# Kernel optimization log

Measured on AMD Instinct MI355X. Metric: run time of the kernel, lower is better.

## Reference

```python
import jax, jax.numpy as jnp
from jax import lax
import numpy as np

S, D, L, H, C = 128, 3, 16, 512, 10
B, T = 32, 16384


def setup_inputs() -> dict:
    key = jax.random.key(0)
    ks = jax.random.split(key, 6)
    x = jax.random.normal(ks[0], (B, D, T), dtype=jnp.float32)
    shapelets = jax.random.normal(ks[1], (S, 1, D, L), dtype=jnp.float32)  # OIHW, one per shapelet
    W1 = jax.random.normal(ks[2], (H, S), dtype=jnp.float32) * (1.0 / np.sqrt(S))
    b1 = jnp.zeros((H,), dtype=jnp.float32)
    W2 = jax.random.normal(ks[3], (C, H), dtype=jnp.float32) * (1.0 / np.sqrt(H))
    b2 = jnp.zeros((C,), dtype=jnp.float32)
    return {"x": x, "shapelets": shapelets, "W1": W1, "b1": b1, "W2": W2, "b2": b2}


def reference(x, shapelets, W1, b1, W2, b2):
    # x: [B, D, T] -> [B, 1, D, T]; kernels slide only over time (full-height conv).
    x4 = x[:, None, :, :]
    dn = ("NCHW", "OIHW", "NCHW")
    ones_k = jnp.ones((1, 1, shapelets.shape[2], shapelets.shape[3]), dtype=x.dtype)
    # ||window||^2 per sliding window: [B, 1, 1, Tout]
    window_square = lax.conv_general_dilated(x4 * x4, ones_k, (1, 1), "VALID", dimension_numbers=dn)
    # all cross-correlations in one grouped conv: [B, S, 1, Tout]
    cross_corr = lax.conv_general_dilated(x4, shapelets, (1, 1), "VALID", dimension_numbers=dn)
    shapelet_square = jnp.sum(shapelets * shapelets, axis=(1, 2, 3))  # [S]
    # squared distance per (shapelet, window), min-reduced over windows
    dist = window_square + shapelet_square[None, :, None, None] - 2.0 * cross_corr  # [B, S, 1, Tout]
    distance = jnp.min(dist, axis=(2, 3))  # [B, S]
    h = jax.nn.relu(distance @ W1.T + b1)
    classification = h @ W2.T + b2
    return (distance, classification)
```

## Files before the change

kernel.cpp:

```cpp
#include <hip/hip_runtime.h>

#define Bn 32
#define Tn 16384
#define Ln 16
#define Sn 128
#define Hn 512
#define Cn 10
#define Kn 48
#define TOUT 16369
#define CH 1024
#define NCH 16
#define XBP 8224

typedef short  s16x8  __attribute__((ext_vector_type(8)));
typedef float  f32x16 __attribute__((ext_vector_type(16)));

static __device__ __forceinline__ unsigned short f2bf(float f) {
    union { float f; unsigned int u; } v; v.f = f;
    unsigned int r = v.u + 0x7FFF + ((v.u >> 16) & 1);
    return (unsigned short)(r >> 16);
}
static __device__ __forceinline__ unsigned int pk(float a, float b) {
    return (unsigned int)f2bf(a) | ((unsigned int)f2bf(b) << 16);
}
static __device__ __forceinline__ unsigned int pk2(unsigned short a, unsigned short b) {
    return (unsigned int)a | ((unsigned int)b << 16);
}
static __device__ __forceinline__ s16x8 mk_a(uint4 t) {
    union { uint4 u; s16x8 v; } c; c.u = t; return c.v;
}

__global__ __launch_bounds__(256) void prep_kernel(const float* __restrict__ x,
                                                   const float* __restrict__ sh,
                                                   unsigned int* __restrict__ shb,
                                                   float* __restrict__ shsq_g,
                                                   float* __restrict__ wsqT,
                                                   unsigned int* __restrict__ xg) {
    const int tid = threadIdx.x;
    if (blockIdx.x == 0) {
        if (tid < Sn) {
            const float4* r4 = (const float4*)(sh + tid * Kn);
            float v[48]; float q = 0.f;
            #pragma unroll
            for (int c = 0; c < 12; ++c) {
                const float4 t = r4[c];
                v[4*c] = t.x; v[4*c+1] = t.y; v[4*c+2] = t.z; v[4*c+3] = t.w;
                q = fmaf(t.x, t.x, q); q = fmaf(t.y, t.y, q);
                q = fmaf(t.z, t.z, q); q = fmaf(t.w, t.w, q);
            }
            shsq_g[tid] = q;
            uint4* dst = (uint4*)(shb + tid * 24);
            #pragma unroll
            for (int c = 0; c < 6; ++c) {
                uint4 o;
                o.x = pk(-2.f*v[8*c  ], -2.f*v[8*c+1]);
                o.y = pk(-2.f*v[8*c+2], -2.f*v[8*c+3]);
                o.z = pk(-2.f*v[8*c+4], -2.f*v[8*c+5]);
                o.w = pk(-2.f*v[8*c+6], -2.f*v[8*c+7]);
                dst[c] = o;
            }
        } else {
            const int idx = tid - 128;
            const uint4 z = {0u, 0u, 0u, 0u};
            for (int r = idx; r < 768; r += 128) {
                uint4* d = (uint4*)(xg + r * XBP + 8192);
                #pragma unroll
                for (int q = 0; q < 8; ++q) d[q] = z;
            }
        }
        return;
    }
    const int bid = blockIdx.x - 1;
    const int b    = bid >> 4;
    const int t0   = ((bid & 15) << 10) + 4 * tid;
    float q[4] = {0.f, 0.f, 0.f, 0.f};
    #pragma unroll
    for (int ch = 0; ch < 3; ++ch) {
        const float* xs = x + (b * 3 + ch) * Tn + t0;
        float wv[20];
        if (t0 + 20 <= Tn) {
            const float4* x4 = (const float4*)xs;
            #pragma unroll
            for (int c = 0; c < 5; ++c) {
                const float4 t = x4[c];
                wv[4*c] = t.x; wv[4*c+1] = t.y; wv[4*c+2] = t.z; wv[4*c+3] = t.w;
            }
        } else {
            #pragma unroll
            for (int k = 0; k < 20; ++k) wv[k] = (t0 + k < Tn) ? xs[k] : 0.f;
        }
        float s = 0.f;
        #pragma unroll
        for (int l = 0; l < 16; ++l) s = fmaf(wv[l], wv[l], s);
        q[0] += s;
        #pragma unroll
        for (int j = 1; j < 4; ++j) {
            s = s - wv[j-1]*wv[j-1] + wv[j+15]*wv[j+15];
            q[j] += s;
        }
        unsigned short bf[20];
        #pragma unroll
        for (int k = 0; k < 20; ++k) bf[k] = f2bf(wv[k]);
        unsigned int* xrow = xg + (b * 24 + ch) * XBP + (t0 >> 1);
        #pragma unroll
        for (int p = 0; p < 8; ++p) {
            uint2 o = { pk2(bf[p], bf[p+1]), pk2(bf[p+2], bf[p+3]) };
            *(uint2*)(xrow + p * 3 * XBP) = o;
        }
    }
    const int r0 = t0 & 15, col = t0 >> 4;
    float* wrow = wsqT + b * (16 * 1024) + col;
    #pragma unroll
    for (int c = 0; c < 4; ++c)
        wrow[(r0 + c) * 1024] = (t0 + c >= TOUT) ? 1e30f : q[c];
}

__global__ __launch_bounds__(256, 3) void dist_kernel(const unsigned int* __restrict__ shb,
                                                      const float* __restrict__ shsq_g,
                                                      const float* __restrict__ wsqT,
                                                      const unsigned int* __restrict__ xg,
                                                      float* __restrict__ partial) {
    __shared__ float wavemin[4 * 64];

    const int tid   = threadIdx.x;
    const int b     = blockIdx.x >> 5;
    const int rem   = blockIdx.x & 31;
    const int chunk = rem >> 1;
    const int half  = rem & 1;
    const int tb    = chunk * CH;
    const int lane  = tid & 63;
    const int w     = tid >> 6;
    const int n     = lane & 31;
    const int h     = lane >> 5;

    s16x8 bfr[3][2];
    float shsqv[2];
    #pragma unroll
    for (int st = 0; st < 2; ++st) {
        const int s = half * 64 + st * 32 + n;
        const uint4* base = (const uint4*)(shb + s * 24);
        #pragma unroll
        for (int kk = 0; kk < 3; ++kk)
            bfr[kk][st] = mk_a(base[kk * 2 + h]);
        shsqv[st] = shsq_g[s];
    }

    float mcol[2] = {1e30f, 1e30f};
    const f32x16 zero16 = {0.f, 0.f, 0.f, 0.f, 0.f, 0.f, 0.f, 0.f,
                           0.f, 0.f, 0.f, 0.f, 0.f, 0.f, 0.f, 0.f};
    const unsigned int* xgb  = xg + b * 24 * XBP + (tb >> 1);
    const float*        wrowb = wsqT + b * (16 * 1024) + (tb >> 4);

    #pragma unroll 2
    for (int rr = 0; rr < 8; ++rr) {
        const int tau = 8 * w + rr;
        const int i   = (tau & 15) + ((tau >> 4) << 9);
        const int p   = i & 7;
        const unsigned int* arow = xgb + p * 3 * XBP + (((i & ~7) >> 1) + 8 * n + 4 * h);
        const s16x8 a0 = mk_a(*(const uint4*)(arow));
        const s16x8 a1 = mk_a(*(const uint4*)(arow + XBP));
        const s16x8 a2 = mk_a(*(const uint4*)(arow + 2 * XBP));

        f32x16 acc[2];
        #pragma unroll
        for (int st = 0; st < 2; ++st) {
            acc[st] = __builtin_amdgcn_mfma_f32_32x32x16_bf16(a0, bfr[0][st], zero16, 0, 0, 0);
            acc[st] = __builtin_amdgcn_mfma_f32_32x32x16_bf16(a1, bfr[1][st], acc[st], 0, 0, 0);
            acc[st] = __builtin_amdgcn_mfma_f32_32x32x16_bf16(a2, bfr[2][st], acc[st], 0, 0, 0);
        }

        const float* wrow = wrowb + (i & 15) * 1024 + ((i >> 9) << 5);
        float4 wq[4];
        #pragma unroll
        for (int q = 0; q < 4; ++q)
            wq[q] = *(const float4*)(wrow + 8 * q + 4 * h);

        #pragma unroll
        for (int st = 0; st < 2; ++st)
            #pragma unroll
            for (int reg = 0; reg < 16; reg += 2) {
                const float u = acc[st][reg]     + ((const float*)&wq[reg >> 2])[(reg & 3)];
                const float v = acc[st][reg + 1] + ((const float*)&wq[reg >> 2])[(reg & 3) + 1];
                mcol[st] = fminf(fminf(mcol[st], u), v);
            }
    }

    #pragma unroll
    for (int st = 0; st < 2; ++st) {
        float mm = mcol[st] + shsqv[st];
        mm = fminf(mm, __shfl_xor(mm, 32, 64));
        if (h == 0) wavemin[w * 64 + st * 32 + n] = mm;
    }
    __syncthreads();
    if (tid < 64) {
        const float mm = fminf(fminf(wavemin[tid], wavemin[64 + tid]),
                               fminf(wavemin[128 + tid], wavemin[192 + tid]));
        partial[(b * NCH + chunk) * Sn + half * 64 + tid] = mm;
    }
}

__global__ __launch_bounds__(512) void mlp_kernel(const float* __restrict__ partial,
                                                  const float* __restrict__ W1,
                                                  const float* __restrict__ b1,
                                                  const float* __restrict__ W2,
                                                  const float* __restrict__ b2,
                                                  float* __restrict__ out) {
    __shared__ float pmin[4][Sn];
    __shared__ float db[Sn];
    __shared__ float hb[Hn];
    __shared__ float part[Cn][32];
    const int b = blockIdx.x, tid = threadIdx.x;

    {
        const int s = tid & 127, g = tid >> 7;
        const float* pp = partial + (b * NCH + g * 4) * Sn + s;
        float m = pp[0];
        #pragma unroll
        for (int c = 1; c < 4; ++c) m = fminf(m, pp[c * Sn]);
        pmin[g][s] = m;
    }
    __syncthreads();
    if (tid < Sn) {
        const float m = fminf(fminf(pmin[0][tid], pmin[1][tid]),
                              fminf(pmin[2][tid], pmin[3][tid]));
        db[tid] = m;
        out[b * Sn + tid] = m;
    }
    __syncthreads();

    float a = b1[tid];
    const float4* w1r = (const float4*)(W1 + tid * Sn);
    const float4* dbv = (const float4*)db;
    #pragma unroll
    for (int i = 0; i < Sn / 4; ++i) {
        const float4 wv = w1r[i];
        const float4 dv = dbv[i];
        a = fmaf(dv.x, wv.x, a); a = fmaf(dv.y, wv.y, a);
        a = fmaf(dv.z, wv.z, a); a = fmaf(dv.w, wv.w, a);
    }
    hb[tid] = fmaxf(a, 0.0f);
    __syncthreads();

    if (tid < Cn * 32) {
        const int c = tid >> 5, p = tid & 31;
        float acc = 0.f;
        #pragma unroll
        for (int i = 0; i < Hn / 32; ++i)
            acc = fmaf(hb[p + 32 * i], W2[c * Hn + p + 32 * i], acc);
        part[c][p] = acc;
    }
    __syncthreads();
    if (tid < Cn) {
        float acc = b2[tid];
        #pragma unroll
        for (int p = 0; p < 32; ++p) acc += part[tid][p];
        out[Bn * Sn + b * Cn + tid] = acc;
    }
}

extern "C" void kernel_launch(void* const* d_in, const int* in_sizes, int n_in,
                              void* d_out, int out_size, void* d_ws, size_t ws_size,
                              hipStream_t stream) {
    const float* x  = (const float*)d_in[0];
    const float* sh = (const float*)d_in[1];
    const float* W1 = (const float*)d_in[2];
    const float* b1 = (const float*)d_in[3];
    const float* W2 = (const float*)d_in[4];
    const float* b2 = (const float*)d_in[5];
    float* out = (float*)d_out;

    char* wsb = (char*)d_ws;
    float*        partial = (float*)wsb;
    unsigned int* shb     = (unsigned int*)(wsb + 262144);
    float*        shsq_g  = (float*)(wsb + 274432);
    float*        wsqT    = (float*)(wsb + 278528);
    unsigned int* xg      = (unsigned int*)(wsb + 2375680);

    prep_kernel<<<513, 256, 0, stream>>>(x, sh, shb, shsq_g, wsqT, xg);
    dist_kernel<<<Bn * NCH * 2, 256, 0, stream>>>(shb, shsq_g, wsqT, xg, partial);
    mlp_kernel<<<Bn, 512, 0, stream>>>(partial, W1, b1, W2, b2, out);
}
```

Measured before the change: 99.74 us.

## Store bf16 input once, fold window-sum into MFMA, split MLP across blocks

The prep kernel now writes a single bf16 copy of each channel instead of eight shifted copies. The dist kernel loads a register window once and builds the odd-shifted operands by funnel shifts. Window and shapelet squared norms are folded into a fourth MFMA as split hi/lo bf16 terms, which removes the per-element fp32 adds. The MLP is spread across four blocks per batch using atomicAdd on outputs pre-filled with b2. This cuts staging traffic and VALU work but adds MFMA work and a small precision risk from the bf16 hi/lo split.

Result: faster. 97.78 us (-2.0%).

```diff
diff --git a/kernel.cpp b/kernel.cpp
--- a/kernel.cpp
+++ b/kernel.cpp
@@ -20,25 +20,37 @@
     unsigned int r = v.u + 0x7FFF + ((v.u >> 16) & 1);
     return (unsigned short)(r >> 16);
 }
+static __device__ __forceinline__ float bf2f(unsigned short b) {
+    union { unsigned int u; float f; } v; v.u = ((unsigned int)b) << 16;
+    return v.f;
+}
 static __device__ __forceinline__ unsigned int pk(float a, float b) {
     return (unsigned int)f2bf(a) | ((unsigned int)f2bf(b) << 16);
 }
 static __device__ __forceinline__ unsigned int pk2(unsigned short a, unsigned short b) {
     return (unsigned int)a | ((unsigned int)b << 16);
 }
-static __device__ __forceinline__ s16x8 mk_a(uint4 t) {
+static __device__ __forceinline__ s16x8 mk_a(unsigned int d0, unsigned int d1,
+                                             unsigned int d2, unsigned int d3) {
+    union { unsigned int u[4]; s16x8 v; } t;
+    t.u[0] = d0; t.u[1] = d1; t.u[2] = d2; t.u[3] = d3;
+    return t.v;
+}
+static __device__ __forceinline__ s16x8 mk_a4(uint4 t) {
     union { uint4 u; s16x8 v; } c; c.u = t; return c.v;
 }
 
 __global__ __launch_bounds__(256) void prep_kernel(const float* __restrict__ x,
                                                    const float* __restrict__ sh,
+                                                   const float* __restrict__ b2,
                                                    unsigned int* __restrict__ shb,
                                                    float* __restrict__ shsq_g,
                                                    float* __restrict__ wsqT,
-                                                   unsigned int* __restrict__ xg) {
+                                                   unsigned int* __restrict__ xbf,
+                                                   float* __restrict__ out) {
     const int tid = threadIdx.x;
     if (blockIdx.x == 0) {
-        if (tid < Sn) {
+        if (tid < 128) {
             const float4* r4 = (const float4*)(sh + tid * Kn);
             float v[48]; float q = 0.f;
             #pragma unroll
@@ -59,20 +71,22 @@
                 o.w = pk(-2.f*v[8*c+6], -2.f*v[8*c+7]);
                 dst[c] = o;
             }
+        } else if (tid < 224) {
+            const int r = tid - 128;
+            uint4* d = (uint4*)(xbf + r * XBP + 8192);
+            const uint4 z = {0u, 0u, 0u, 0u};
+            #pragma unroll
+            for (int q = 0; q < 8; ++q) d[q] = z;
         } else {
-            const int idx = tid - 128;
-            const uint4 z = {0u, 0u, 0u, 0u};
-            for (int r = idx; r < 768; r += 128) {
-                uint4* d = (uint4*)(xg + r * XBP + 8192);
-                #pragma unroll
-                for (int q = 0; q < 8; ++q) d[q] = z;
-            }
+            const int k0 = (tid - 224) * 10;
+            #pragma unroll
+            for (int c = 0; c < Cn; ++c) out[Bn * Sn + k0 + c] = b2[c];
         }
         return;
     }
     const int bid = blockIdx.x - 1;
-    const int b    = bid >> 4;
-    const int t0   = ((bid & 15) << 10) + 4 * tid;
+    const int b   = bid >> 4;
+    const int t0  = ((bid & 15) << 10) + 4 * tid;
     float q[4] = {0.f, 0.f, 0.f, 0.f};
     #pragma unroll
     for (int ch = 0; ch < 3; ++ch) {
@@ -98,18 +112,11 @@
             s = s - wv[j-1]*wv[j-1] + wv[j+15]*wv[j+15];
             q[j] += s;
         }
-        unsigned short bf[20];
-        #pragma unroll
-        for (int k = 0; k < 20; ++k) bf[k] = f2bf(wv[k]);
-        unsigned int* xrow = xg + (b * 24 + ch) * XBP + (t0 >> 1);
-        #pragma unroll
-        for (int p = 0; p < 8; ++p) {
-            uint2 o = { pk2(bf[p], bf[p+1]), pk2(bf[p+2], bf[p+3]) };
-            *(uint2*)(xrow + p * 3 * XBP) = o;
-        }
+        uint2 o = { pk(wv[0], wv[1]), pk(wv[2], wv[3]) };
+        *(uint2*)(xbf + (b * 3 + ch) * XBP + (t0 >> 1)) = o;
     }
     const int r0 = t0 & 15, col = t0 >> 4;
-    float* wrow = wsqT + b * (16 * 1024) + col;
+    float* wrow = wsqT + b * 16384 + col;
     #pragma unroll
     for (int c = 0; c < 4; ++c)
         wrow[(r0 + c) * 1024] = (t0 + c >= TOUT) ? 1e30f : q[c];
@@ -118,7 +125,7 @@
 __global__ __launch_bounds__(256, 3) void dist_kernel(const unsigned int* __restrict__ shb,
                                                       const float* __restrict__ shsq_g,
                                                       const float* __restrict__ wsqT,
-                                                      const unsigned int* __restrict__ xg,
+                                                      const unsigned int* __restrict__ xbf,
                                                       float* __restrict__ partial) {
     __shared__ float wavemin[4 * 64];
 
@@ -133,61 +140,80 @@
     const int n     = lane & 31;
     const int h     = lane >> 5;
 
-    s16x8 bfr[3][2];
-    float shsqv[2];
+    s16x8 bfr[3][2], b4[2];
     #pragma unroll
     for (int st = 0; st < 2; ++st) {
         const int s = half * 64 + st * 32 + n;
         const uint4* base = (const uint4*)(shb + s * 24);
         #pragma unroll
-        for (int kk = 0; kk < 3; ++kk)
-            bfr[kk][st] = mk_a(base[kk * 2 + h]);
-        shsqv[st] = shsq_g[s];
+        for (int kk = 0; kk < 3; ++kk) {
+            const uint4 t = base[kk * 2 + h];
+            bfr[kk][st] = mk_a(t.x, t.y, t.z, t.w);
+        }
+        const float q = shsq_g[s];
+        const unsigned short qh = f2bf(q);
+        const unsigned short ql = f2bf(q - bf2f(qh));
+        b4[st] = h ? mk_a(0u, 0u, 0u, 0u)
+                   : mk_a(0x3F803F80u, pk2(qh, ql), 0u, 0u);
+    }
+
+    unsigned int u[3][8];
+    {
+        const int D0 = (tb >> 1) + 4 * (w & 1) + ((w >> 1) << 8) + 8 * n + 4 * h;
+        #pragma unroll
+        for (int ch = 0; ch < 3; ++ch) {
+            const unsigned int* xr = xbf + (b * 3 + ch) * XBP + D0;
+            const uint4 lo = *(const uint4*)(xr);
+            const uint4 hi = *(const uint4*)(xr + 4);
+            u[ch][0] = lo.x; u[ch][1] = lo.y; u[ch][2] = lo.z; u[ch][3] = lo.w;
+            u[ch][4] = hi.x; u[ch][5] = hi.y; u[ch][6] = hi.z; u[ch][7] = hi.w;
+        }
     }
 
     float mcol[2] = {1e30f, 1e30f};
     const f32x16 zero16 = {0.f, 0.f, 0.f, 0.f, 0.f, 0.f, 0.f, 0.f,
                            0.f, 0.f, 0.f, 0.f, 0.f, 0.f, 0.f, 0.f};
-    const unsigned int* xgb  = xg + b * 24 * XBP + (tb >> 1);
-    const float*        wrowb = wsqT + b * (16 * 1024) + (tb >> 4);
-
-    #pragma unroll 2
+    const int   base_t = 8 * (w & 1) + ((w >> 1) << 9);
+    const float* wbase = wsqT + b * 16384 + (tb >> 4) + n;
+
+    #pragma unroll
     for (int rr = 0; rr < 8; ++rr) {
-        const int tau = 8 * w + rr;
-        const int i   = (tau & 15) + ((tau >> 4) << 9);
-        const int p   = i & 7;
-        const unsigned int* arow = xgb + p * 3 * XBP + (((i & ~7) >> 1) + 8 * n + 4 * h);
-        const s16x8 a0 = mk_a(*(const uint4*)(arow));
-        const s16x8 a1 = mk_a(*(const uint4*)(arow + XBP));
-        const s16x8 a2 = mk_a(*(const uint4*)(arow + 2 * XBP));
-
-        f32x16 acc[2];
+        const int i = base_t + rr;
+        s16x8 a[3];
+        #pragma unroll
+        for (int ch = 0; ch < 3; ++ch) {
+            if ((rr & 1) == 0) {
+                a[ch] = mk_a(u[ch][rr/2], u[ch][rr/2+1], u[ch][rr/2+2], u[ch][rr/2+3]);
+            } else {
+                unsigned int d[4];
+                #pragma unroll
+                for (int k = 0; k < 4; ++k)
+                    d[k] = (u[ch][rr/2 + k] >> 16) | (u[ch][rr/2 + k + 1] << 16);
+                a[ch] = mk_a(d[0], d[1], d[2], d[3]);
+            }
+        }
+        const float wv = wbase[(i & 15) * 1024 + ((i >> 9) << 5)];
+        const unsigned short wh = f2bf(wv);
+        const unsigned short wl = f2bf(wv - bf2f(wh));
+        const s16x8 a4 = h ? mk_a(0u, 0u, 0u, 0u)
+                           : mk_a(pk2(wh, wl), 0x3F803F80u, 0u, 0u);
+
         #pragma unroll
         for (int st = 0; st < 2; ++st) {
-            acc[st] = __builtin_amdgcn_mfma_f32_32x32x16_bf16(a0, bfr[0][st], zero16, 0, 0, 0);
-            acc[st] = __builtin_amdgcn_mfma_f32_32x32x16_bf16(a1, bfr[1][st], acc[st], 0, 0, 0);
-            acc[st] = __builtin_amdgcn_mfma_f32_32x32x16_bf16(a2, bfr[2][st], acc[st], 0, 0, 0);
-        }
-
-        const float* wrow = wrowb + (i & 15) * 1024 + ((i >> 9) << 5);
-        float4 wq[4];
-        #pragma unroll
-        for (int q = 0; q < 4; ++q)
-            wq[q] = *(const float4*)(wrow + 8 * q + 4 * h);
-
-        #pragma unroll
-        for (int st = 0; st < 2; ++st)
-            #pragma unroll
-            for (int reg = 0; reg < 16; reg += 2) {
-                const float u = acc[st][reg]     + ((const float*)&wq[reg >> 2])[(reg & 3)];
-                const float v = acc[st][reg + 1] + ((const float*)&wq[reg >> 2])[(reg & 3) + 1];
-                mcol[st] = fminf(fminf(mcol[st], u), v);
-            }
+            f32x16 acc;
+            acc = __builtin_amdgcn_mfma_f32_32x32x16_bf16(a[0], bfr[0][st], zero16, 0, 0, 0);
+            acc = __builtin_amdgcn_mfma_f32_32x32x16_bf16(a[1], bfr[1][st], acc, 0, 0, 0);
+            acc = __builtin_amdgcn_mfma_f32_32x32x16_bf16(a[2], bfr[2][st], acc, 0, 0, 0);
+            acc = __builtin_amdgcn_mfma_f32_32x32x16_bf16(a4,   b4[st],    acc, 0, 0, 0);
+            #pragma unroll
+            for (int reg = 0; reg < 16; reg += 2)
+                mcol[st] = fminf(fminf(mcol[st], acc[reg]), acc[reg + 1]);
+        }
     }
 
     #pragma unroll
     for (int st = 0; st < 2; ++st) {
-        float mm = mcol[st] + shsqv[st];
+        float mm = mcol[st];
         mm = fminf(mm, __shfl_xor(mm, 32, 64));
         if (h == 0) wavemin[w * 64 + st * 32 + n] = mm;
     }
@@ -203,58 +229,60 @@
                                                   const float* __restrict__ W1,
                                                   const float* __restrict__ b1,
                                                   const float* __restrict__ W2,
-                                                  const float* __restrict__ b2,
                                                   float* __restrict__ out) {
     __shared__ float pmin[4][Sn];
     __shared__ float db[Sn];
-    __shared__ float hb[Hn];
+    __shared__ float hb[128];
     __shared__ float part[Cn][32];
-    const int b = blockIdx.x, tid = threadIdx.x;
+    const int b = blockIdx.x >> 2, g = blockIdx.x & 3, tid = threadIdx.x;
 
     {
-        const int s = tid & 127, g = tid >> 7;
-        const float* pp = partial + (b * NCH + g * 4) * Sn + s;
+        const int s = tid & 127, cg = tid >> 7;
+        const float* pp = partial + (b * NCH + cg * 4) * Sn + s;
         float m = pp[0];
         #pragma unroll
         for (int c = 1; c < 4; ++c) m = fminf(m, pp[c * Sn]);
-        pmin[g][s] = m;
+        pmin[cg][s] = m;
     }
     __syncthreads();
     if (tid < Sn) {
         const float m = fminf(fminf(pmin[0][tid], pmin[1][tid]),
                               fminf(pmin[2][tid], pmin[3][tid]));
         db[tid] = m;
-        out[b * Sn + tid] = m;
-    }
-    __syncthreads();
-
-    float a = b1[tid];
-    const float4* w1r = (const float4*)(W1 + tid * Sn);
-    const float4* dbv = (const float4*)db;
-    #pragma unroll
-    for (int i = 0; i < Sn / 4; ++i) {
-        const float4 wv = w1r[i];
-        const float4 dv = dbv[i];
-        a = fmaf(dv.x, wv.x, a); a = fmaf(dv.y, wv.y, a);
-        a = fmaf(dv.z, wv.z, a); a = fmaf(dv.w, wv.w, a);
-    }
-    hb[tid] = fmaxf(a, 0.0f);
+        if (g == 0) out[b * Sn + tid] = m;
+    }
+    __syncthreads();
+
+    if (tid < 128) {
+        const int hrow = g * 128 + tid;
+        float a = b1[hrow];
+        const float4* w1r = (const float4*)(W1 + hrow * Sn);
+        const float4* dbv = (const float4*)db;
+        #pragma unroll
+        for (int i = 0; i < Sn / 4; ++i) {
+            const float4 wv = w1r[i];
+            const float4 dv = dbv[i];
+            a = fmaf(dv.x, wv.x, a); a = fmaf(dv.y, wv.y, a);
+            a = fmaf(dv.z, wv.z, a); a = fmaf(dv.w, wv.w, a);
+        }
+        hb[tid] = fmaxf(a, 0.0f);
+    }
     __syncthreads();
 
     if (tid < Cn * 32) {
         const int c = tid >> 5, p = tid & 31;
         float acc = 0.f;
         #pragma unroll
-        for (int i = 0; i < Hn / 32; ++i)
-            acc = fmaf(hb[p + 32 * i], W2[c * Hn + p + 32 * i], acc);
+        for (int k = 0; k < 4; ++k)
+            acc = fmaf(hb[p + 32 * k], W2[c * Hn + g * 128 + p + 32 * k], acc);
         part[c][p] = acc;
     }
     __syncthreads();
     if (tid < Cn) {
-        float acc = b2[tid];
+        float acc = 0.f;
         #pragma unroll
         for (int p = 0; p < 32; ++p) acc += part[tid][p];
-        out[Bn * Sn + b * Cn + tid] = acc;
+        atomicAdd(&out[Bn * Sn + b * Cn + tid], acc);
     }
 }
 
@@ -274,9 +302,9 @@
     unsigned int* shb     = (unsigned int*)(wsb + 262144);
     float*        shsq_g  = (float*)(wsb + 274432);
     float*        wsqT    = (float*)(wsb + 278528);
-    unsigned int* xg      = (unsigned int*)(wsb + 2375680);
-
-    prep_kernel<<<513, 256, 0, stream>>>(x, sh, shb, shsq_g, wsqT, xg);
-    dist_kernel<<<Bn * NCH * 2, 256, 0, stream>>>(shb, shsq_g, wsqT, xg, partial);
-    mlp_kernel<<<Bn, 512, 0, stream>>>(partial, W1, b1, W2, b2, out);
-}
+    unsigned int* xbf     = (unsigned int*)(wsb + 2375680);
+
+    prep_kernel<<<513, 256, 0, stream>>>(x, sh, b2, shb, shsq_g, wsqT, xbf, out);
+    dist_kernel<<<Bn * NCH * 2, 256, 0, stream>>>(shb, shsq_g, wsqT, xbf, partial);
+    mlp_kernel<<<Bn * 4, 512, 0, stream>>>(partial, W1, b1, W2, out);
+}
```
